# Kernel optimization log

Measured on AMD Instinct MI355X. Metric: run time of the kernel, lower is better.

## Reference

```python
import jax, jax.numpy as jnp
import numpy as np

TEMP = 0.1
EPS = 1e-12


def _l2_normalize(x):
    n = jnp.sqrt(jnp.sum(x * x, axis=1, keepdims=True))
    return x / jnp.maximum(n, EPS)


def _unif(x, t=2.0):
    # log-mean of exp(-t * squared pairwise distances), over unordered pairs (torch.pdist)
    g = x @ x.T                       # [n, n] gram
    sq = jnp.diagonal(g)
    d2 = jnp.maximum(sq[:, None] + sq[None, :] - 2.0 * g, 0.0)
    n = x.shape[0]
    iu = jnp.triu(jnp.ones((n, n), dtype=bool), k=1)
    s = jnp.where(iu, jnp.exp(-t * d2), 0.0).sum()
    return jnp.log(s / (n * (n - 1) / 2))


def setup_inputs() -> dict:
    key = jax.random.key(0)
    k1, k2 = jax.random.split(key)
    B, D = 4096, 1024
    return {
        "proj_1": jax.random.normal(k1, (B, D), dtype=jnp.float32),
        "proj_2": jax.random.normal(k2, (B, D), dtype=jnp.float32),
    }


def reference(proj_1, proj_2):
    B = proj_1.shape[0]
    z_i = _l2_normalize(proj_1)
    z_j = _l2_normalize(proj_2)
    z = jnp.concatenate([z_i, z_j], axis=0)          # [2B, D]
    # cosine similarity of unit vectors == dot product (normalize + GEMM)
    sim = z @ z.T                                     # [2B, 2B]

    idx = jnp.arange(B)
    sim_ij = sim[idx, idx + B]                        # diag(sim, +B)
    sim_ji = sim[idx + B, idx]                        # diag(sim, -B)
    positives = jnp.concatenate([sim_ij, sim_ji], axis=0)  # [2B]

    mask = ~jnp.eye(2 * B, dtype=bool)
    denom = jnp.where(mask, jnp.exp(sim / TEMP), 0.0).sum(axis=1)  # [2B]
    all_losses = -(positives / TEMP - jnp.log(denom))
    loss = all_losses.sum() / (2 * B)

    lalign = jax.lax.stop_gradient(
        jnp.mean(jnp.sum((z_i - z_j) ** 2, axis=1))   # ||.||_2^alpha with alpha=2
    )
    half = B // 2
    lunif = jax.lax.stop_gradient(
        (_unif(z_i[:half]) + _unif(z_i[half:])) / 2.0
    )
    return loss, lalign, lunif
```

## Files before the change

### kernel.cpp

```cpp
#include <hip/hip_runtime.h>
#include <hip/hip_bf16.h>
#include <math.h>

#define DIM 1024
#define NB  4096
#define N2  8192
#define BT  256
#define NT2 32
#define PS  34
#define GRID_FULL 512
#define GRID_ALL  576

#define C1f 8.9447146e-4f
#define C2f 3.5778876e-4f
#define C2b (-5.7707802f)

typedef int i32x4 __attribute__((ext_vector_type(4)));

__device__ __forceinline__ void gload_lds16(const unsigned char* g, unsigned char* l) {
    __builtin_amdgcn_global_load_lds((__attribute__((address_space(1))) void*)(g),
                                     (__attribute__((address_space(3))) void*)(l),
                                     16, 0, 0);
}

__device__ __forceinline__ unsigned int pk4_i8(float a, float b, float c, float d) {
    const int ia = __float2int_rn(a * 127.0f), ib = __float2int_rn(b * 127.0f);
    const int ic = __float2int_rn(c * 127.0f), id = __float2int_rn(d * 127.0f);
    return (unsigned)(ia & 255) | ((unsigned)(ib & 255) << 8) |
           ((unsigned)(ic & 255) << 16) | ((unsigned)(id & 255) << 24);
}

__global__ __launch_bounds__(256) void norm_kernel(
    const float* __restrict__ p1, const float* __restrict__ p2,
    unsigned char* __restrict__ zq, float* __restrict__ pos)
{
    const int r = blockIdx.x;
    const int t = threadIdx.x;
    const float4 x1 = ((const float4*)(p1 + (size_t)r * DIM))[t];
    const float4 x2 = ((const float4*)(p2 + (size_t)r * DIM))[t];
    float s1  = x1.x*x1.x + x1.y*x1.y + x1.z*x1.z + x1.w*x1.w;
    float s2  = x2.x*x2.x + x2.y*x2.y + x2.z*x2.z + x2.w*x2.w;
    float s12 = x1.x*x2.x + x1.y*x2.y + x1.z*x2.z + x1.w*x2.w;
#pragma unroll
    for (int off = 1; off < 64; off <<= 1) {
        s1  += __shfl_xor(s1,  off);
        s2  += __shfl_xor(s2,  off);
        s12 += __shfl_xor(s12, off);
    }
    __shared__ float ls[3][4];
    const int wid = t >> 6;
    if ((t & 63) == 0) { ls[0][wid] = s1; ls[1][wid] = s2; ls[2][wid] = s12; }
    __syncthreads();
    s1  = ls[0][0] + ls[0][1] + ls[0][2] + ls[0][3];
    s2  = ls[1][0] + ls[1][1] + ls[1][2] + ls[1][3];
    s12 = ls[2][0] + ls[2][1] + ls[2][2] + ls[2][3];
    const float rn1 = 1.0f / fmaxf(sqrtf(s1), 1e-12f);
    const float rn2 = 1.0f / fmaxf(sqrtf(s2), 1e-12f);
    if (t == 0) pos[r] = s12 * rn1 * rn2;

    const int j0 = (t << 2) & 63;
    const int kb = t >> 4;
    const int pb = (j0 < 32) ? (((j0 >> 3) << 4) + (j0 & 7))
                             : ((((j0 - 32) >> 3) << 4) + 8 + ((j0 - 32) & 7));
    const size_t off8 = (size_t)kb * 64 + pb;
    *(unsigned int*)(zq + (size_t)r * DIM + off8) =
        pk4_i8(x1.x * rn1, x1.y * rn1, x1.z * rn1, x1.w * rn1);
    *(unsigned int*)(zq + (size_t)(NB + r) * DIM + off8) =
        pk4_i8(x2.x * rn2, x2.y * rn2, x2.z * rn2, x2.w * rn2);
}

__global__ __launch_bounds__(1024, 4) void sim_kernel(
    const unsigned char* __restrict__ zq,
    float* __restrict__ partials,
    float* __restrict__ lup)
{
    __shared__ __align__(16) unsigned char buf[2][2][BT * 128];
    const int t    = threadIdx.x;
    const int lane = t & 63;
    const int wid  = t >> 6;
    const int fr   = lane & 15;
    const int kg   = lane >> 4;
    const int cb0  = ((kg ^ (fr & 7)) << 4);
    const int sgr8 = (((lane & 7) ^ ((lane >> 3) & 7)) << 4);
    const int rsub = (lane >> 4) << 2;
    const int csub = lane & 15;
    const int bid = blockIdx.x;

    if (bid < GRID_FULL) {
        int jj = (bid & 7) * 64 + (bid >> 3);
#pragma unroll 1
        for (int k = 16; k < 32; ++k) {
            const int e = k * 32 - ((k * (k - 1)) >> 1);
            if (jj >= e) ++jj;
        }
        int rt = 0;
        while ((rt + 1) * 32 - (((rt + 1) * rt) >> 1) <= jj) ++rt;
        const int ct = rt + jj - (rt * 32 - ((rt * (rt - 1)) >> 1));
        const bool isdiag = (rt == ct);
        const int row0 = rt << 8;
        const int col0 = ct << 8;
        const int wr = wid >> 2;
        const int wc = wid & 3;

        const int abase = ((wr << 6) + fr) << 7;
        const int bbase = ((wc << 6) + fr) << 7;

        const int ar0 = row0 + ((wid << 1) << 3) + (lane >> 3);
        const int br0 = col0 + ((wid << 1) << 3) + (lane >> 3);
        const unsigned char* asrc = zq + (size_t)ar0 * DIM + sgr8;
        const unsigned char* bsrc = zq + (size_t)br0 * DIM + sgr8;

#define STAGEF(bsel, kp) do { \
        gload_lds16(asrc + (kp) * 128,              &buf[bsel][0][(wid << 11)]); \
        gload_lds16(asrc + (size_t)8 * DIM + (kp) * 128, &buf[bsel][0][(wid << 11) + 1024]); \
        gload_lds16(bsrc + (kp) * 128,              &buf[bsel][1][(wid << 11)]); \
        gload_lds16(bsrc + (size_t)8 * DIM + (kp) * 128, &buf[bsel][1][(wid << 11) + 1024]); \
    } while (0)

        i32x4 acc[4][4] = {};
        STAGEF(0, 0);
        __syncthreads();

#pragma unroll
        for (int kp = 0; kp < 8; ++kp) {
            const int cur = kp & 1;
            if (kp < 7) STAGEF(cur ^ 1, kp + 1);
            const unsigned char* Ab = &buf[cur][0][0] + abase;
            const unsigned char* Bb = &buf[cur][1][0] + bbase;
#pragma unroll
            for (int h = 0; h < 2; ++h) {
                const int cbh = cb0 ^ (h << 6);
                i32x4 bq[4];
#pragma unroll
                for (int n = 0; n < 4; ++n)
                    bq[n] = *(const i32x4*)(Bb + (n << 11) + cbh);
#pragma unroll
                for (int m = 0; m < 4; ++m) {
                    const i32x4 aq = *(const i32x4*)(Ab + (m << 11) + cbh);
#pragma unroll
                    for (int n = 0; n < 4; ++n)
                        acc[m][n] = __builtin_amdgcn_mfma_i32_16x16x64_i8(aq, bq[n], acc[m][n], 0, 0, 0);
                }
            }
            __syncthreads();
        }
#undef STAGEF

        float* rsum4 = (float*)&buf[0][0][0];
        float* csum4 = rsum4 + 1024;
        float* lured = csum4 + 1024;
        const bool inreg = (ct < 8) || (rt >= 8 && ct < 16);
        const int  rbase = row0 + (wr << 6);
        const int  cbase = col0 + (wc << 6);

        float lu = 0.0f;
        float cs[4] = {0.0f, 0.0f, 0.0f, 0.0f};
#pragma unroll
        for (int m = 0; m < 4; ++m) {
            float rs[4] = {0.0f, 0.0f, 0.0f, 0.0f};
#pragma unroll
            for (int n = 0; n < 4; ++n) {
                const int gcol = cbase + (n << 4) + csub;
#pragma unroll
                for (int r = 0; r < 4; ++r) {
                    const int grow = rbase + (m << 4) + rsub + r;
                    const float f = (float)acc[m][n][r];
                    float e = exp2f(f * C1f);
                    if (isdiag) e = (grow != gcol) ? e : 0.0f;
                    rs[r] += e;
                    cs[n] += e;
                    if (inreg && (!isdiag || gcol > grow))
                        lu += exp2f(fmaf(f, C2f, C2b));
                }
            }
#pragma unroll
            for (int off = 1; off < 16; off <<= 1) {
#pragma unroll
                for (int r = 0; r < 4; ++r) rs[r] += __shfl_xor(rs[r], off);
            }
            if ((lane & 15) == 0) {
#pragma unroll
                for (int r = 0; r < 4; ++r)
                    rsum4[((wr << 6) + (m << 4) + rsub + r) * 4 + wc] = rs[r];
            }
        }
        if (!isdiag) {
#pragma unroll
            for (int off = 16; off < 64; off <<= 1) {
#pragma unroll
                for (int n = 0; n < 4; ++n) cs[n] += __shfl_xor(cs[n], off);
            }
            if (lane < 16) {
#pragma unroll
                for (int n = 0; n < 4; ++n)
                    csum4[((wc << 6) + (n << 4) + lane) * 4 + wr] = cs[n];
            }
        }
#pragma unroll
        for (int off = 1; off < 64; off <<= 1) lu += __shfl_xor(lu, off);
        if (lane == 0) lured[wid] = lu;
        __syncthreads();

        if (t == 0) {
            float s = 0.0f;
#pragma unroll
            for (int w = 0; w < 16; ++w) s += lured[w];
            lup[rt * NT2 + ct] = s;
        }
        if (t < 256) {
            const float* p = rsum4 + t * 4;
            partials[(size_t)(row0 + t) * PS + ct] = ((p[0] + p[1]) + p[2]) + p[3];
        } else if (t < 512 && !isdiag) {
            const float* p = csum4 + (t - 256) * 4;
            partials[(size_t)(col0 + t - 256) * PS + rt] = ((p[0] + p[1]) + p[2]) + p[3];
        }
    } else {
        const int q  = bid - GRID_FULL;
        const int k  = 16 + (q >> 2);
        const int qr = (q >> 1) & 1;
        const int qc = q & 1;
        const int row0 = (k << 8) + (qr << 7);
        const int col0 = (k << 8) + (qc << 7);
        const int wr = wid >> 2;
        const int wc = wid & 3;

        const int ch  = wid << 1;
        const int isB = ch >> 4;
        const int chl = ch & 15;
        const unsigned char* spanel =
            zq + (size_t)((isB ? col0 : row0) + (chl << 3) + (lane >> 3)) * DIM + sgr8;
        unsigned char* d0a = &buf[0][isB][chl << 10];
        unsigned char* d1a = &buf[1][isB][chl << 10];

        i32x4 acc[2][2] = {};
        gload_lds16(spanel, d0a);
        gload_lds16(spanel + (size_t)8 * DIM, d0a + 1024);
        __syncthreads();

#pragma unroll
        for (int kp = 0; kp < 8; ++kp) {
            const int cur = kp & 1;
            if (kp < 7) {
                unsigned char* dn = cur ? d0a : d1a;
                gload_lds16(spanel + (kp + 1) * 128, dn);
                gload_lds16(spanel + (size_t)8 * DIM + (kp + 1) * 128, dn + 1024);
            }
            const unsigned char* Ab = &buf[cur][0][0] + (((wr << 5) + fr) << 7);
            const unsigned char* Bb = &buf[cur][1][0] + (((wc << 5) + fr) << 7);
#pragma unroll
            for (int h = 0; h < 2; ++h) {
                const int cbh = cb0 ^ (h << 6);
                i32x4 aq[2], bq[2];
#pragma unroll
                for (int n = 0; n < 2; ++n)
                    bq[n] = *(const i32x4*)(Bb + (n << 11) + cbh);
#pragma unroll
                for (int m = 0; m < 2; ++m)
                    aq[m] = *(const i32x4*)(Ab + (m << 11) + cbh);
#pragma unroll
                for (int m = 0; m < 2; ++m)
#pragma unroll
                    for (int n = 0; n < 2; ++n)
                        acc[m][n] = __builtin_amdgcn_mfma_i32_16x16x64_i8(aq[m], bq[n], acc[m][n], 0, 0, 0);
            }
            __syncthreads();
        }

        float* rsum4 = (float*)&buf[0][0][0];
#pragma unroll
        for (int m = 0; m < 2; ++m) {
            float rs[4] = {0.0f, 0.0f, 0.0f, 0.0f};
#pragma unroll
            for (int n = 0; n < 2; ++n) {
                const int gcol = col0 + (wc << 5) + (n << 4) + csub;
#pragma unroll
                for (int r = 0; r < 4; ++r) {
                    const int grow = row0 + (wr << 5) + (m << 4) + rsub + r;
                    float e = exp2f((float)acc[m][n][r] * C1f);
                    e = (grow != gcol) ? e : 0.0f;
                    rs[r] += e;
                }
            }
#pragma unroll
            for (int off = 1; off < 16; off <<= 1) {
#pragma unroll
                for (int r = 0; r < 4; ++r) rs[r] += __shfl_xor(rs[r], off);
            }
            if ((lane & 15) == 0) {
#pragma unroll
                for (int r = 0; r < 4; ++r)
                    rsum4[((wr << 5) + (m << 4) + rsub + r) * 4 + wc] = rs[r];
            }
        }
        __syncthreads();
        if (t < 128) {
            const float* p = rsum4 + t * 4;
            partials[(size_t)(row0 + t) * PS + (qc ? 32 : k)] =
                ((p[0] + p[1]) + p[2]) + p[3];
        }
    }
}

__global__ __launch_bounds__(128) void logred_kernel(
    const float* __restrict__ partials, double* __restrict__ red_log)
{
    const int t   = threadIdx.x;
    const int row = blockIdx.x * 128 + t;
    const float* p = partials + (size_t)row * PS;
    float dsum = 0.0f;
#pragma unroll
    for (int i = 0; i < 33; ++i) dsum += p[i];
    double l = log((double)dsum);
    __shared__ double sd[128];
    sd[t] = l;
    __syncthreads();
    for (int s = 64; s > 0; s >>= 1) {
        if (t < s) sd[t] += sd[t + s];
        __syncthreads();
    }
    if (t == 0) red_log[blockIdx.x] = sd[0];
}

__global__ __launch_bounds__(256) void final_kernel(
    const double* __restrict__ red_log, const float* __restrict__ pos,
    const float* __restrict__ lup, float* __restrict__ out)
{
    const int t = threadIdx.x;
    double dlog = 0.0, dpos = 0.0, ds1 = 0.0, ds2 = 0.0;
    if (t < 64) dlog = red_log[t];
    for (int i = t; i < NB; i += 256) dpos += (double)pos[i];
    for (int i = t; i < NT2 * NT2; i += 256) {
        const int rt = i >> 5, ct = i & 31;
        if (rt > ct) continue;
        const double v = (double)lup[i];
        if (rt < 8 && ct < 8) ds1 += v;
        else if (rt >= 8 && rt < 16 && ct >= 8 && ct < 16) ds2 += v;
    }
    __shared__ double sd[4][256];
    sd[0][t] = dlog; sd[1][t] = dpos; sd[2][t] = ds1; sd[3][t] = ds2;
    __syncthreads();
    for (int s = 128; s > 0; s >>= 1) {
        if (t < s) {
            sd[0][t] += sd[0][t + s]; sd[1][t] += sd[1][t + s];
            sd[2][t] += sd[2][t + s]; sd[3][t] += sd[3][t + s];
        }
        __syncthreads();
    }
    if (t == 0) {
        const double mean_pos = sd[1][0] / (double)NB;
        const double loss   = sd[0][0] / (double)N2 - mean_pos * 10.0;
        const double lalign = 2.0 - 2.0 * mean_pos;
        const double C      = 2048.0 * 2047.0 * 0.5;
        const double lunif  = 0.5 * (log(sd[2][0] / C) + log(sd[3][0] / C));
        out[0] = (float)loss;
        out[1] = (float)lalign;
        out[2] = (float)lunif;
    }
}

extern "C" void kernel_launch(void* const* d_in, const int* in_sizes, int n_in,
                              void* d_out, int out_size, void* d_ws, size_t ws_size,
                              hipStream_t stream) {
    const float* p1 = (const float*)d_in[0];
    const float* p2 = (const float*)d_in[1];
    float* out = (float*)d_out;

    char* ws = (char*)d_ws;
    unsigned char* zq = (unsigned char*)ws;
    float*  partials  = (float*)(ws + ((size_t)8 << 20));
    float*  pos       = (float*)(ws + ((size_t)10 << 20));
    float*  lup       = (float*)(ws + ((size_t)10 << 20) + 16384);
    double* red_log   = (double*)(ws + ((size_t)10 << 20) + 16384 + 4096);

    hipMemsetAsync(partials, 0, (size_t)N2 * PS * sizeof(float), stream);
    hipLaunchKernelGGL(norm_kernel,   dim3(NB),       dim3(256),  0, stream, p1, p2, zq, pos);
    hipLaunchKernelGGL(sim_kernel,    dim3(GRID_ALL), dim3(1024), 0, stream, zq, partials, lup);
    hipLaunchKernelGGL(logred_kernel, dim3(64),       dim3(128),  0, stream, partials, red_log);
    hipLaunchKernelGGL(final_kernel,  dim3(1),        dim3(256),  0, stream, red_log, pos, lup, out);
}
```

Before: 79.71 us.

## Load B operand fragments directly from global memory instead of staging in LDS

The int8 GEMM tiles now stage only the A panel through LDS. Each wave reads its B fragments straight from global memory into registers inside the k-loop, in both the full-tile and diagonal-quarter paths. This halves LDS usage and LDS write traffic, which may allow more blocks per CU. The trade-off is that B loads become per-wave global reads with latency exposed inside the MFMA loop and repeated across the waves sharing a column, so performance relies on L1/L2 hits.

```diff
diff --git a/kernel.cpp b/kernel.cpp
--- a/kernel.cpp
+++ b/kernel.cpp
@@ -74,7 +74,7 @@
     float* __restrict__ partials,
     float* __restrict__ lup)
 {
-    __shared__ __align__(16) unsigned char buf[2][2][BT * 128];
+    __shared__ __align__(16) unsigned char buf[2][BT * 128];
     const int t    = threadIdx.x;
     const int lane = t & 63;
     const int wid  = t >> 6;
@@ -103,37 +103,34 @@
         const int wc = wid & 3;
 
         const int abase = ((wr << 6) + fr) << 7;
-        const int bbase = ((wc << 6) + fr) << 7;
-
-        const int ar0 = row0 + ((wid << 1) << 3) + (lane >> 3);
-        const int br0 = col0 + ((wid << 1) << 3) + (lane >> 3);
-        const unsigned char* asrc = zq + (size_t)ar0 * DIM + sgr8;
-        const unsigned char* bsrc = zq + (size_t)br0 * DIM + sgr8;
-
-#define STAGEF(bsel, kp) do { \
-        gload_lds16(asrc + (kp) * 128,              &buf[bsel][0][(wid << 11)]); \
-        gload_lds16(asrc + (size_t)8 * DIM + (kp) * 128, &buf[bsel][0][(wid << 11) + 1024]); \
-        gload_lds16(bsrc + (kp) * 128,              &buf[bsel][1][(wid << 11)]); \
-        gload_lds16(bsrc + (size_t)8 * DIM + (kp) * 128, &buf[bsel][1][(wid << 11) + 1024]); \
+
+        const unsigned char* asrc =
+            zq + (size_t)(row0 + (wid << 4) + (lane >> 3)) * DIM + sgr8;
+        const unsigned char* bptr =
+            zq + (size_t)(col0 + (wc << 6) + fr) * DIM + (kg << 4);
+
+#define STAGEA(bsel, kp) do { \
+        gload_lds16(asrc + (kp) * 128,                   &buf[bsel][(wid << 11)]); \
+        gload_lds16(asrc + (size_t)8 * DIM + (kp) * 128, &buf[bsel][(wid << 11) + 1024]); \
     } while (0)
 
         i32x4 acc[4][4] = {};
-        STAGEF(0, 0);
+        STAGEA(0, 0);
         __syncthreads();
 
 #pragma unroll
         for (int kp = 0; kp < 8; ++kp) {
             const int cur = kp & 1;
-            if (kp < 7) STAGEF(cur ^ 1, kp + 1);
-            const unsigned char* Ab = &buf[cur][0][0] + abase;
-            const unsigned char* Bb = &buf[cur][1][0] + bbase;
+            if (kp < 7) STAGEA(cur ^ 1, kp + 1);
+            const unsigned char* Ab = &buf[cur][0] + abase;
+            const unsigned char* bk = bptr + kp * 128;
 #pragma unroll
             for (int h = 0; h < 2; ++h) {
                 const int cbh = cb0 ^ (h << 6);
                 i32x4 bq[4];
 #pragma unroll
                 for (int n = 0; n < 4; ++n)
-                    bq[n] = *(const i32x4*)(Bb + (n << 11) + cbh);
+                    bq[n] = *(const i32x4*)(bk + (size_t)(n << 4) * DIM + (h << 6));
 #pragma unroll
                 for (int m = 0; m < 4; ++m) {
                     const i32x4 aq = *(const i32x4*)(Ab + (m << 11) + cbh);
@@ -144,9 +141,9 @@
             }
             __syncthreads();
         }
-#undef STAGEF
-
-        float* rsum4 = (float*)&buf[0][0][0];
+#undef STAGEA
+
+        float* rsum4 = (float*)&buf[0][0];
         float* csum4 = rsum4 + 1024;
         float* lured = csum4 + 1024;
         const bool inreg = (ct < 8) || (rt >= 8 && ct < 16);
@@ -224,36 +221,28 @@
         const int wr = wid >> 2;
         const int wc = wid & 3;
 
-        const int ch  = wid << 1;
-        const int isB = ch >> 4;
-        const int chl = ch & 15;
-        const unsigned char* spanel =
-            zq + (size_t)((isB ? col0 : row0) + (chl << 3) + (lane >> 3)) * DIM + sgr8;
-        unsigned char* d0a = &buf[0][isB][chl << 10];
-        unsigned char* d1a = &buf[1][isB][chl << 10];
+        const unsigned char* asrc =
+            zq + (size_t)(row0 + (wid << 3) + (lane >> 3)) * DIM + sgr8;
+        const unsigned char* bptr =
+            zq + (size_t)(col0 + (wc << 5) + fr) * DIM + (kg << 4);
 
         i32x4 acc[2][2] = {};
-        gload_lds16(spanel, d0a);
-        gload_lds16(spanel + (size_t)8 * DIM, d0a + 1024);
+        gload_lds16(asrc, &buf[0][wid << 10]);
         __syncthreads();
 
 #pragma unroll
         for (int kp = 0; kp < 8; ++kp) {
             const int cur = kp & 1;
-            if (kp < 7) {
-                unsigned char* dn = cur ? d0a : d1a;
-                gload_lds16(spanel + (kp + 1) * 128, dn);
-                gload_lds16(spanel + (size_t)8 * DIM + (kp + 1) * 128, dn + 1024);
-            }
-            const unsigned char* Ab = &buf[cur][0][0] + (((wr << 5) + fr) << 7);
-            const unsigned char* Bb = &buf[cur][1][0] + (((wc << 5) + fr) << 7);
+            if (kp < 7) gload_lds16(asrc + (kp + 1) * 128, &buf[cur ^ 1][wid << 10]);
+            const unsigned char* Ab = &buf[cur][0] + (((wr << 5) + fr) << 7);
+            const unsigned char* bk = bptr + kp * 128;
 #pragma unroll
             for (int h = 0; h < 2; ++h) {
                 const int cbh = cb0 ^ (h << 6);
                 i32x4 aq[2], bq[2];
 #pragma unroll
                 for (int n = 0; n < 2; ++n)
-                    bq[n] = *(const i32x4*)(Bb + (n << 11) + cbh);
+                    bq[n] = *(const i32x4*)(bk + (size_t)(n << 4) * DIM + (h << 6));
 #pragma unroll
                 for (int m = 0; m < 2; ++m)
                     aq[m] = *(const i32x4*)(Ab + (m << 11) + cbh);
@@ -266,7 +255,7 @@
             __syncthreads();
         }
 
-        float* rsum4 = (float*)&buf[0][0][0];
+        float* rsum4 = (float*)&buf[0][0];
 #pragma unroll
         for (int m = 0; m < 2; ++m) {
             float rs[4] = {0.0f, 0.0f, 0.0f, 0.0f};
```

Measured after the change: 131.4 us. 64.8% more time.
